# Kernel tuning notes

Hardware: AMD Instinct MI355X
Metric: run time of the kernel (lower is better)

Reference implementation:

```python
import jax, jax.numpy as jnp
import numpy as np

C_IN, C_P1, C_G1, N_OUT = 512, 256, 256, 6
B, H, W = 256, 19, 19


def mish(x):
    return x * jnp.tanh(jax.nn.softplus(x))


def setup_inputs() -> dict:
    key = jax.random.key(0)
    ks = jax.random.split(key, 8)
    x = jax.random.normal(ks[0], (B, C_IN, H, W), dtype=jnp.float32)
    mask = jnp.ones((B, 1, H, W), dtype=jnp.float32)
    conv1p_w = jax.random.normal(ks[1], (C_P1, C_IN), dtype=jnp.float32) * (1.0 / np.sqrt(C_IN))
    conv1g_w = jax.random.normal(ks[2], (C_G1, C_IN), dtype=jnp.float32) * (1.0 / np.sqrt(C_IN))
    beta_g = jnp.zeros((C_G1,), dtype=jnp.float32)
    linear_g_w = jax.random.normal(ks[3], (C_P1, 3 * C_G1), dtype=jnp.float32) * (1.0 / np.sqrt(3 * C_G1))
    beta2 = jnp.zeros((C_P1,), dtype=jnp.float32)
    conv2p_w = jax.random.normal(ks[4], (N_OUT, C_P1), dtype=jnp.float32) * (0.3 / np.sqrt(C_P1))
    return {"x": x, "mask": mask, "conv1p_w": conv1p_w, "conv1g_w": conv1g_w,
            "beta_g": beta_g, "linear_g_w": linear_g_w, "beta2": beta2, "conv2p_w": conv2p_w}


def reference(x, mask, conv1p_w, conv1g_w, beta_g, linear_g_w, beta2, conv2p_w):
    # 1x1 convs are channel GEMMs
    outp = jnp.einsum('bchw,oc->bohw', x, conv1p_w)              # [B, C_P1, H, W]
    outg = jnp.einsum('bchw,oc->bohw', x, conv1g_w)              # [B, C_G1, H, W]
    # BiasMask (scale=None) + Mish
    outg = mish((outg + beta_g[None, :, None, None]) * mask)
    # KataGPool: mean, scaled mean, max (masked)
    mask_sum_hw = jnp.sum(mask, axis=(2, 3), keepdims=True)      # [B,1,1,1]
    layer_mean = jnp.sum(outg * mask, axis=(2, 3), keepdims=True) / mask_sum_hw
    layer_max = jnp.max(outg + (mask - 1.0), axis=(2, 3), keepdims=True)
    sqrt_off = (jnp.sqrt(mask_sum_hw) - 14.0) / 10.0
    pooled = jnp.concatenate([layer_mean, layer_mean * sqrt_off, layer_max], axis=1)  # [B, 3*C_G1, 1, 1]
    pooled = pooled[:, :, 0, 0]                                  # [B, 3*C_G1]
    g = pooled @ linear_g_w.T                                    # [B, C_P1]
    # broadcast-add, BiasMask, Mish
    outp = mish((outp + g[:, :, None, None] + beta2[None, :, None, None]) * mask)
    # final 1x1 conv + invalid-move penalty
    outp = jnp.einsum('bchw,oc->bohw', outp, conv2p_w)           # [B, 6, H, W]
    outp = outp - (1.0 - mask) * 5000.0
    return outp.reshape(outp.shape[0], outp.shape[1], -1)        # [B, 6, H*W]
```

## Files before the change

kernel.cpp:

```cpp
#include <hip/hip_runtime.h>
#include <math.h>

#define BATCH 256
#define CIN   512
#define CP    256
#define HW    361
#define NOUT  6
#define NT    6

typedef short bf16x8 __attribute__((ext_vector_type(8)));
typedef float f32x4  __attribute__((ext_vector_type(4)));

__device__ __forceinline__ short f2bf(float f) {
    unsigned u = __float_as_uint(f);
    u += 0x7fffu + ((u >> 16) & 1u);
    return (short)(u >> 16);
}
__device__ __forceinline__ float bf2f(short s) {
    return __uint_as_float(((unsigned)(unsigned short)s) << 16);
}
__device__ __forceinline__ float mish_f(float v) {
    float u = __expf(v);
    float a = 1.f + u;
    float w = a * a;
    float r = v * (w - 1.f) * __builtin_amdgcn_rcpf(w + 1.f);
    return (v > 30.f) ? v : r;
}
__device__ __forceinline__ void gl_lds16(const void* g, void* l) {
    __builtin_amdgcn_global_load_lds(
        (const __attribute__((address_space(1))) void*)g,
        (__attribute__((address_space(3))) void*)l, 16, 0, 0);
}

__global__ __launch_bounds__(256) void k0_weights(
    const float* __restrict__ w1p, const float* __restrict__ w1g,
    short* __restrict__ wT)
{
    int g = blockIdx.x * 256 + threadIdx.x;
    int kb  = g >> 11;
    int row = (g >> 2) & 511;
    int s   = g & 3;
    int sc  = s ^ ((row >> 1) & 3);
    const float* src = (row < 256) ? (w1p + (size_t)row * CIN)
                                   : (w1g + (size_t)(row - 256) * CIN);
    int c = kb * 32 + sc * 8;
    float f[8];
    *(float4*)(f)     = *(const float4*)(src + c);
    *(float4*)(f + 4) = *(const float4*)(src + c + 4);
    bf16x8 v;
    #pragma unroll
    for (int i = 0; i < 8; ++i) v[i] = f2bf(f[i]);
    *(bf16x8*)((char*)wT + (size_t)kb * 32768 + row * 64 + s * 16) = v;
}

__global__ __launch_bounds__(512, 4) void k1_conv1(
    const float* __restrict__ x, const short* __restrict__ wT,
    const float* __restrict__ mask, const float* __restrict__ beta_g,
    short* __restrict__ outp_pre, float* __restrict__ psum, float* __restrict__ pmax)
{
    int orig = blockIdx.x;
    int newid = (orig & 7) * 192 + (orig >> 3);
    int n = newid % NT;
    int b = newid / NT;

    const int tid = threadIdx.x;
    const int lane = tid & 63, wid = tid >> 6;
    const int lc = lane & 15, lg = lane >> 4;
    const int hw0 = n * 64;

    __shared__ __align__(16) short As[2][16384];
    __shared__ __align__(16) short Bs[2][2048];
    __shared__ float maskS[64];
    __shared__ float betaS[256];

    if (tid < 64) {
        int hwg_ = hw0 + tid;
        maskS[tid] = (hwg_ < HW) ? mask[b * HW + hwg_] : 0.f;
    }
    if (tid < 256) betaS[tid] = beta_g[tid];
    asm volatile("s_waitcnt vmcnt(0) lgkmcnt(0)" ::: "memory");
    __builtin_amdgcn_sched_barrier(0);

    const bool bduty = tid < 256;
    const int brow = tid & 63;
    const int bs   = (tid >> 6) & 3;
    const int hwg  = hw0 + brow;
    const bool bvalid = bduty && (hwg < HW);
    const float* xb = x + ((size_t)b * CIN + bs * 8) * HW + hwg;
    const int bDstOff = brow * 64 + ((bs ^ ((brow >> 1) & 3)) * 16);
    char* bDstBase = (char*)Bs;

    const char* aSrc = (const char*)wT + tid * 16;
    char* aDst = (char*)As + tid * 16;

    int aOff[4], bOff[4];
    #pragma unroll
    for (int mf = 0; mf < 4; ++mf) {
        int r = wid * 64 + mf * 16 + lc;
        aOff[mf] = r * 64 + ((lg ^ ((r >> 1) & 3)) * 16);
    }
    #pragma unroll
    for (int nf = 0; nf < 4; ++nf) {
        int r = nf * 16 + lc;
        bOff[nf] = r * 64 + ((lg ^ ((r >> 1) & 3)) * 16);
    }

    float regB[8];
    #pragma unroll
    for (int i = 0; i < 8; ++i) regB[i] = 0.f;

    f32x4 acc[4][4];
    #pragma unroll
    for (int i = 0; i < 4; ++i)
        #pragma unroll
        for (int j = 0; j < 4; ++j)
            acc[i][j] = (f32x4){0.f, 0.f, 0.f, 0.f};

#define BLOAD(kb)                                                          \
    do {                                                                   \
        if (bduty) {                                                       \
            const float* src_ = xb + (size_t)(kb) * 32 * HW;               \
            _Pragma("unroll")                                              \
            for (int i_ = 0; i_ < 8; ++i_)                                 \
                regB[i_] = bvalid ? src_[(size_t)i_ * HW] : 0.f;           \
        }                                                                  \
    } while (0)

#define BWRITE(buf)                                                        \
    do {                                                                   \
        if (bduty) {                                                       \
            bf16x8 o_;                                                     \
            _Pragma("unroll")                                              \
            for (int i_ = 0; i_ < 8; ++i_) o_[i_] = f2bf(regB[i_]);        \
            *(bf16x8*)(bDstBase + (buf) * 4096 + bDstOff) = o_;            \
        }                                                                  \
    } while (0)

#define ALOAD(buf, kb)                                                     \
    do {                                                                   \
        _Pragma("unroll")                                                  \
        for (int l_ = 0; l_ < 4; ++l_)                                     \
            gl_lds16(aSrc + (size_t)(kb) * 32768 + l_ * 8192,              \
                     aDst + (buf) * 32768 + l_ * 8192);                    \
    } while (0)

    BLOAD(0);
    ALOAD(0, 0);
    asm volatile("s_waitcnt vmcnt(4)" ::: "memory");
    __builtin_amdgcn_sched_barrier(0);
    BWRITE(0);
    asm volatile("s_waitcnt vmcnt(0) lgkmcnt(0)" ::: "memory");
    __builtin_amdgcn_s_barrier();
    __builtin_amdgcn_sched_barrier(0);

    #pragma unroll
    for (int t = 0; t < 16; ++t) {
        const char* ab = (const char*)As + (t & 1) * 32768;
        const char* bb = (const char*)Bs + (t & 1) * 4096;

        bf16x8 aF[4], bF[4];
        #pragma unroll
        for (int mf = 0; mf < 4; ++mf) aF[mf] = *(const bf16x8*)(ab + aOff[mf]);
        #pragma unroll
        for (int nf = 0; nf < 4; ++nf) bF[nf] = *(const bf16x8*)(bb + bOff[nf]);

        if (t < 15) {
            BLOAD(t + 1);
            ALOAD((t + 1) & 1, t + 1);
        }

        __builtin_amdgcn_s_setprio(1);
        #pragma unroll
        for (int mf = 0; mf < 4; ++mf)
            #pragma unroll
            for (int nf = 0; nf < 4; ++nf)
                acc[mf][nf] = __builtin_amdgcn_mfma_f32_16x16x32_bf16(
                    aF[mf], bF[nf], acc[mf][nf], 0, 0, 0);
        __builtin_amdgcn_s_setprio(0);

        if (t < 15) {
            asm volatile("s_waitcnt vmcnt(4)" ::: "memory");
            __builtin_amdgcn_sched_barrier(0);
            BWRITE((t + 1) & 1);
            asm volatile("s_waitcnt vmcnt(0) lgkmcnt(0)" ::: "memory");
            __builtin_amdgcn_s_barrier();
            __builtin_amdgcn_sched_barrier(0);
        }
    }

    if (wid < 4) {
        #pragma unroll
        for (int mf = 0; mf < 4; ++mf) {
            int ch = wid * 64 + mf * 16 + lg * 4;
            #pragma unroll
            for (int nf = 0; nf < 4; ++nf) {
                int hw = hw0 + nf * 16 + lc;
                if (hw < HW) {
                    #pragma unroll
                    for (int j = 0; j < 4; ++j)
                        outp_pre[((size_t)(b * CP + ch + j)) * HW + hw] = f2bf(acc[mf][nf][j]);
                }
            }
        }
    } else {
        #pragma unroll
        for (int mf = 0; mf < 4; ++mf) {
            #pragma unroll
            for (int j = 0; j < 4; ++j) {
                int rloc = (wid - 4) * 64 + mf * 16 + lg * 4 + j;
                float beta = betaS[rloc];
                float s = 0.f, mx = -INFINITY;
                #pragma unroll
                for (int nf = 0; nf < 4; ++nf) {
                    int cl = nf * 16 + lc;
                    int hw = hw0 + cl;
                    float mv = maskS[cl];
                    float val = mish_f((acc[mf][nf][j] + beta) * mv);
                    if (hw < HW) {
                        s += val * mv;
                        mx = fmaxf(mx, val + mv - 1.f);
                    }
                }
                #pragma unroll
                for (int off = 1; off < 16; off <<= 1) {
                    s += __shfl_xor(s, off, 64);
                    mx = fmaxf(mx, __shfl_xor(mx, off, 64));
                }
                if (lc == 0) {
                    psum[((size_t)(b * CP + rloc)) * NT + n] = s;
                    pmax[((size_t)(b * CP + rloc)) * NT + n] = mx;
                }
            }
        }
    }
#undef BLOAD
#undef BWRITE
#undef ALOAD
}

__global__ __launch_bounds__(256) void k2_pool_linear(
    const float* __restrict__ mask, const float* __restrict__ psum,
    const float* __restrict__ pmax, const float* __restrict__ lw,
    float* __restrict__ g_out)
{
    int b = blockIdx.x, t = threadIdx.x;
    __shared__ float pooled[768];
    __shared__ float msr[4];

    float s = 0.f;
    for (int i = t; i < HW; i += 256) s += mask[b * HW + i];
    #pragma unroll
    for (int off = 1; off < 64; off <<= 1) s += __shfl_xor(s, off, 64);
    if ((t & 63) == 0) msr[t >> 6] = s;
    __syncthreads();
    float msum = msr[0] + msr[1] + msr[2] + msr[3];

    {
        int c = t;
        const float* ps = psum + (size_t)(b * CP + c) * NT;
        const float* pm = pmax + (size_t)(b * CP + c) * NT;
        float s3 = 0.f, m3 = -INFINITY;
        #pragma unroll
        for (int i = 0; i < NT; ++i) { s3 += ps[i]; m3 = fmaxf(m3, pm[i]); }
        float mean = s3 / msum;
        float sq = (sqrtf(msum) - 14.f) * 0.1f;
        pooled[c] = mean; pooled[256 + c] = mean * sq; pooled[512 + c] = m3;
    }
    __syncthreads();
    {
        int o = t;
        const float4* wrow = (const float4*)(lw + (size_t)o * 768);
        float acc = 0.f;
        #pragma unroll 8
        for (int j = 0; j < 192; ++j) {
            float4 w4 = wrow[j];
            float4 p4 = *(const float4*)&pooled[j * 4];
            acc += p4.x * w4.x + p4.y * w4.y + p4.z * w4.z + p4.w * w4.w;
        }
        g_out[b * CP + o] = acc;
    }
}

__global__ __launch_bounds__(256) void k3_final(
    const short* __restrict__ outp_pre, const float* __restrict__ mask,
    const float* __restrict__ g_out, const float* __restrict__ beta2,
    const float* __restrict__ w2, float* __restrict__ out)
{
    int ht = blockIdx.x, b = blockIdx.y;
    int t = threadIdx.x;
    __shared__ float w2S[NOUT * 256];
    __shared__ float gbS[256];
    __shared__ float part[NOUT][256];

    for (int i = t; i < NOUT * 256; i += 256) w2S[i] = w2[i];
    gbS[t] = g_out[b * CP + t] + beta2[t];
    __syncthreads();

    int hw = t & 63, cg = t >> 6;
    int hwg = ht * 64 + hw;
    bool valid = hwg < HW;
    float maskv = valid ? mask[b * HW + hwg] : 0.f;

    float acc[NOUT] = {0.f, 0.f, 0.f, 0.f, 0.f, 0.f};
    const short* src = outp_pre + ((size_t)(b * CP + cg * 64)) * HW + hwg;
    #pragma unroll 4
    for (int ci = 0; ci < 64; ++ci) {
        float v = valid ? bf2f(src[(size_t)ci * HW]) : 0.f;
        float mm = mish_f((v + gbS[cg * 64 + ci]) * maskv);
        #pragma unroll
        for (int o = 0; o < NOUT; ++o) acc[o] += mm * w2S[o * 256 + cg * 64 + ci];
    }
    #pragma unroll
    for (int o = 0; o < NOUT; ++o) part[o][t] = acc[o];
    __syncthreads();

    for (int idx = t; idx < NOUT * 64; idx += 256) {
        int o = idx >> 6, h2 = idx & 63;
        int hg = ht * 64 + h2;
        if (hg < HW) {
            float mv = mask[b * HW + hg];
            float sum = part[o][h2] + part[o][64 + h2] + part[o][128 + h2] + part[o][192 + h2];
            out[((size_t)(b * NOUT + o)) * HW + hg] = sum - (1.f - mv) * 5000.f;
        }
    }
}

extern "C" void kernel_launch(void* const* d_in, const int* in_sizes, int n_in,
                              void* d_out, int out_size, void* d_ws, size_t ws_size,
                              hipStream_t stream) {
    const float* x     = (const float*)d_in[0];
    const float* mask  = (const float*)d_in[1];
    const float* w1p   = (const float*)d_in[2];
    const float* w1g   = (const float*)d_in[3];
    const float* betag = (const float*)d_in[4];
    const float* lw    = (const float*)d_in[5];
    const float* beta2 = (const float*)d_in[6];
    const float* w2    = (const float*)d_in[7];
    float* out = (float*)d_out;

    char* ws = (char*)d_ws;
    short* outp_pre = (short*)(ws);
    short* wT       = (short*)(ws + 47316992);
    float* psum     = (float*)(ws + 47841280);
    float* pmax     = (float*)(ws + 49414144);
    float* g_out    = (float*)(ws + 50987008);

    hipLaunchKernelGGL(k0_weights, dim3(128), dim3(256), 0, stream, w1p, w1g, wT);
    hipLaunchKernelGGL(k1_conv1, dim3(1536), dim3(512), 0, stream,
                       x, wT, mask, betag, outp_pre, psum, pmax);
    hipLaunchKernelGGL(k2_pool_linear, dim3(BATCH), dim3(256), 0, stream,
                       mask, psum, pmax, lw, g_out);
    hipLaunchKernelGGL(k3_final, dim3(6, BATCH), dim3(256), 0, stream,
                       outp_pre, mask, g_out, beta2, w2, out);
    (void)in_sizes; (void)n_in; (void)out_size; (void)ws_size;
}
```

Before: 145.5 us.

## Spread x loads across all waves and prefetch B tile two steps ahead

Each of the eight waves now loads four fp32 input channels for the B tile, where before only the first four waves loaded eight each. Register double-buffering lets the global x loads run two k-steps ahead of their LDS write, so the barrier no longer waits on all outstanding loads each iteration. The aim is to hide global load latency for the strided x reads behind the MFMA work. The cost is more registers and a more intricate vmcnt accounting, which must stay correct across the A loads that go directly into LDS.

```diff
diff --git a/kernel.cpp b/kernel.cpp
--- a/kernel.cpp
+++ b/kernel.cpp
@@ -9,6 +9,7 @@
 #define NT    6
 
 typedef short bf16x8 __attribute__((ext_vector_type(8)));
+typedef short bf16x4 __attribute__((ext_vector_type(4)));
 typedef float f32x4  __attribute__((ext_vector_type(4)));
 
 __device__ __forceinline__ short f2bf(float f) {
@@ -81,13 +82,12 @@
     asm volatile("s_waitcnt vmcnt(0) lgkmcnt(0)" ::: "memory");
     __builtin_amdgcn_sched_barrier(0);
 
-    const bool bduty = tid < 256;
     const int brow = tid & 63;
-    const int bs   = (tid >> 6) & 3;
+    const int q    = tid >> 6;
     const int hwg  = hw0 + brow;
-    const bool bvalid = bduty && (hwg < HW);
-    const float* xb = x + ((size_t)b * CIN + bs * 8) * HW + hwg;
-    const int bDstOff = brow * 64 + ((bs ^ ((brow >> 1) & 3)) * 16);
+    const bool bvalid = hwg < HW;
+    const float* xq = x + ((size_t)b * CIN + q * 4) * HW + hwg;
+    const int bDstOff = brow * 64 + (((q >> 1) ^ ((brow >> 1) & 3)) * 16) + ((q & 1) * 8);
     char* bDstBase = (char*)Bs;
 
     const char* aSrc = (const char*)wT + tid * 16;
@@ -105,9 +105,9 @@
         bOff[nf] = r * 64 + ((lg ^ ((r >> 1) & 3)) * 16);
     }
 
-    float regB[8];
-    #pragma unroll
-    for (int i = 0; i < 8; ++i) regB[i] = 0.f;
+    float regB[2][4];
+    #pragma unroll
+    for (int i = 0; i < 4; ++i) { regB[0][i] = 0.f; regB[1][i] = 0.f; }
 
     f32x4 acc[4][4];
     #pragma unroll
@@ -116,24 +116,20 @@
         for (int j = 0; j < 4; ++j)
             acc[i][j] = (f32x4){0.f, 0.f, 0.f, 0.f};
 
-#define BLOAD(kb)                                                          \
+#define BLOAD(SET, kb)                                                     \
     do {                                                                   \
-        if (bduty) {                                                       \
-            const float* src_ = xb + (size_t)(kb) * 32 * HW;               \
-            _Pragma("unroll")                                              \
-            for (int i_ = 0; i_ < 8; ++i_)                                 \
-                regB[i_] = bvalid ? src_[(size_t)i_ * HW] : 0.f;           \
-        }                                                                  \
+        const float* src_ = xq + (size_t)(kb) * 32 * HW;                   \
+        _Pragma("unroll")                                                  \
+        for (int i_ = 0; i_ < 4; ++i_)                                     \
+            regB[SET][i_] = bvalid ? src_[(size_t)i_ * HW] : 0.f;          \
     } while (0)
 
-#define BWRITE(buf)                                                        \
+#define BWRITE(SET, buf)                                                   \
     do {                                                                   \
-        if (bduty) {                                                       \
-            bf16x8 o_;                                                     \
-            _Pragma("unroll")                                              \
-            for (int i_ = 0; i_ < 8; ++i_) o_[i_] = f2bf(regB[i_]);        \
-            *(bf16x8*)(bDstBase + (buf) * 4096 + bDstOff) = o_;            \
-        }                                                                  \
+        bf16x4 o_;                                                         \
+        _Pragma("unroll")                                                  \
+        for (int i_ = 0; i_ < 4; ++i_) o_[i_] = f2bf(regB[SET][i_]);       \
+        *(bf16x4*)(bDstBase + (buf) * 4096 + bDstOff) = o_;                \
     } while (0)
 
 #define ALOAD(buf, kb)                                                     \
@@ -144,12 +140,15 @@
                      aDst + (buf) * 32768 + l_ * 8192);                    \
     } while (0)
 
-    BLOAD(0);
+    BLOAD(0, 0);
     ALOAD(0, 0);
     asm volatile("s_waitcnt vmcnt(4)" ::: "memory");
     __builtin_amdgcn_sched_barrier(0);
-    BWRITE(0);
-    asm volatile("s_waitcnt vmcnt(0) lgkmcnt(0)" ::: "memory");
+    BWRITE(0, 0);
+    BLOAD(1, 1);
+    asm volatile("s_waitcnt vmcnt(4)" ::: "memory");
+    __builtin_amdgcn_sched_barrier(0);
+    asm volatile("s_waitcnt lgkmcnt(0)" ::: "memory");
     __builtin_amdgcn_s_barrier();
     __builtin_amdgcn_sched_barrier(0);
 
@@ -164,10 +163,8 @@
         #pragma unroll
         for (int nf = 0; nf < 4; ++nf) bF[nf] = *(const bf16x8*)(bb + bOff[nf]);
 
-        if (t < 15) {
-            BLOAD(t + 1);
-            ALOAD((t + 1) & 1, t + 1);
-        }
+        if (t < 15) ALOAD((t + 1) & 1, t + 1);
+        if (t < 14) BLOAD(t & 1, t + 2);
 
         __builtin_amdgcn_s_setprio(1);
         #pragma unroll
@@ -179,10 +176,14 @@
         __builtin_amdgcn_s_setprio(0);
 
         if (t < 15) {
-            asm volatile("s_waitcnt vmcnt(4)" ::: "memory");
+            if (t < 14) {
+                asm volatile("s_waitcnt vmcnt(4)" ::: "memory");
+            } else {
+                asm volatile("s_waitcnt vmcnt(0)" ::: "memory");
+            }
             __builtin_amdgcn_sched_barrier(0);
-            BWRITE((t + 1) & 1);
-            asm volatile("s_waitcnt vmcnt(0) lgkmcnt(0)" ::: "memory");
+            BWRITE((t + 1) & 1, (t + 1) & 1);
+            asm volatile("s_waitcnt lgkmcnt(0)" ::: "memory");
             __builtin_amdgcn_s_barrier();
             __builtin_amdgcn_sched_barrier(0);
         }
```

Result: faster. 141.7 us (median of 4 runs) (-2.6%).

## Load conv1 weights directly into registers and widen K tile to 64

Applied to the files above, without the earlier changes.

The conv1 GEMM stops staging the weight (A) tile in LDS via global_load_lds and instead has each wave read its weight fragments straight from global memory into registers, with a simpler row-major weight layout. The x (B) tile now covers 64 input channels per step, loaded by all 512 threads into a larger swizzled LDS buffer, which halves the number of K iterations and barriers. The intent is to free LDS, cut barrier and LDS traffic, and rely on L2 reuse of the weights. The trade-off is that weight loads go through registers with higher latency exposure and more redundant global reads across blocks.

```diff
diff --git a/kernel.cpp b/kernel.cpp
--- a/kernel.cpp
+++ b/kernel.cpp
@@ -26,31 +26,24 @@
     float r = v * (w - 1.f) * __builtin_amdgcn_rcpf(w + 1.f);
     return (v > 30.f) ? v : r;
 }
-__device__ __forceinline__ void gl_lds16(const void* g, void* l) {
-    __builtin_amdgcn_global_load_lds(
-        (const __attribute__((address_space(1))) void*)g,
-        (__attribute__((address_space(3))) void*)l, 16, 0, 0);
-}
 
 __global__ __launch_bounds__(256) void k0_weights(
     const float* __restrict__ w1p, const float* __restrict__ w1g,
     short* __restrict__ wT)
 {
     int g = blockIdx.x * 256 + threadIdx.x;
-    int kb  = g >> 11;
-    int row = (g >> 2) & 511;
-    int s   = g & 3;
-    int sc  = s ^ ((row >> 1) & 3);
+    int row = g >> 6;
+    int ck  = g & 63;
     const float* src = (row < 256) ? (w1p + (size_t)row * CIN)
                                    : (w1g + (size_t)(row - 256) * CIN);
-    int c = kb * 32 + sc * 8;
+    int c = ck * 8;
     float f[8];
     *(float4*)(f)     = *(const float4*)(src + c);
     *(float4*)(f + 4) = *(const float4*)(src + c + 4);
     bf16x8 v;
     #pragma unroll
     for (int i = 0; i < 8; ++i) v[i] = f2bf(f[i]);
-    *(bf16x8*)((char*)wT + (size_t)kb * 32768 + row * 64 + s * 16) = v;
+    *(bf16x8*)((char*)wT + (size_t)row * 1024 + ck * 16) = v;
 }
 
 __global__ __launch_bounds__(512, 4) void k1_conv1(
@@ -68,8 +61,7 @@
     const int lc = lane & 15, lg = lane >> 4;
     const int hw0 = n * 64;
 
-    __shared__ __align__(16) short As[2][16384];
-    __shared__ __align__(16) short Bs[2][2048];
+    __shared__ __align__(16) short Bs[2][4096];
     __shared__ float maskS[64];
     __shared__ float betaS[256];
 
@@ -78,31 +70,24 @@
         maskS[tid] = (hwg_ < HW) ? mask[b * HW + hwg_] : 0.f;
     }
     if (tid < 256) betaS[tid] = beta_g[tid];
-    asm volatile("s_waitcnt vmcnt(0) lgkmcnt(0)" ::: "memory");
-    __builtin_amdgcn_sched_barrier(0);
-
-    const bool bduty = tid < 256;
+
     const int brow = tid & 63;
-    const int bs   = (tid >> 6) & 3;
+    const int q    = tid >> 6;
     const int hwg  = hw0 + brow;
-    const bool bvalid = bduty && (hwg < HW);
-    const float* xb = x + ((size_t)b * CIN + bs * 8) * HW + hwg;
-    const int bDstOff = brow * 64 + ((bs ^ ((brow >> 1) & 3)) * 16);
+    const bool bvalid = hwg < HW;
+    const float* xq = x + ((size_t)b * CIN + q * 8) * HW + hwg;
+    const int bDstOff = brow * 128 + ((q ^ ((brow >> 1) & 7)) * 16);
     char* bDstBase = (char*)Bs;
 
-    const char* aSrc = (const char*)wT + tid * 16;
-    char* aDst = (char*)As + tid * 16;
-
-    int aOff[4], bOff[4];
-    #pragma unroll
-    for (int mf = 0; mf < 4; ++mf) {
-        int r = wid * 64 + mf * 16 + lc;
-        aOff[mf] = r * 64 + ((lg ^ ((r >> 1) & 3)) * 16);
-    }
+    const char* aBase = (const char*)wT + (size_t)(wid * 64 + lc) * 1024 + lg * 16;
+
+    int bOff[4][2];
     #pragma unroll
     for (int nf = 0; nf < 4; ++nf) {
         int r = nf * 16 + lc;
-        bOff[nf] = r * 64 + ((lg ^ ((r >> 1) & 3)) * 16);
+        #pragma unroll
+        for (int kh = 0; kh < 2; ++kh)
+            bOff[nf][kh] = r * 128 + (((kh * 4 + lg) ^ ((r >> 1) & 7)) * 16);
     }
 
     float regB[8];
@@ -118,71 +103,65 @@
 
 #define BLOAD(kb)                                                          \
     do {                                                                   \
-        if (bduty) {                                                       \
-            const float* src_ = xb + (size_t)(kb) * 32 * HW;               \
-            _Pragma("unroll")                                              \
-            for (int i_ = 0; i_ < 8; ++i_)                                 \
-                regB[i_] = bvalid ? src_[(size_t)i_ * HW] : 0.f;           \
-        }                                                                  \
+        const float* src_ = xq + (size_t)(kb) * 64 * HW;                   \
+        _Pragma("unroll")                                                  \
+        for (int i_ = 0; i_ < 8; ++i_)                                     \
+            regB[i_] = bvalid ? src_[(size_t)i_ * HW] : 0.f;               \
     } while (0)
 
 #define BWRITE(buf)                                                        \
     do {                                                                   \
-        if (bduty) {                                                       \
-            bf16x8 o_;                                                     \
+        bf16x8 o_;                                                         \
+        _Pragma("unroll")                                                  \
+        for (int i_ = 0; i_ < 8; ++i_) o_[i_] = f2bf(regB[i_]);            \
+        *(bf16x8*)(bDstBase + (buf) * 8192 + bDstOff) = o_;                \
+    } while (0)
+
+#define ALOAD(dst, kb, kh)                                                 \
+    do {                                                                   \
+        _Pragma("unroll")                                                  \
+        for (int mf_ = 0; mf_ < 4; ++mf_)                                  \
+            dst[mf_] = *(const bf16x8*)(aBase + mf_ * 16384 +              \
+                                        (kb) * 128 + (kh) * 64);           \
+    } while (0)
+
+#define MFMA_HALF(af, buf, kh)                                             \
+    do {                                                                   \
+        bf16x8 bF_[4];                                                     \
+        _Pragma("unroll")                                                  \
+        for (int nf_ = 0; nf_ < 4; ++nf_)                                  \
+            bF_[nf_] = *(const bf16x8*)((const char*)Bs + (buf) * 8192 +   \
+                                        bOff[nf_][kh]);                    \
+        __builtin_amdgcn_s_setprio(1);                                     \
+        _Pragma("unroll")                                                  \
+        for (int mf_ = 0; mf_ < 4; ++mf_)                                  \
             _Pragma("unroll")                                              \
-            for (int i_ = 0; i_ < 8; ++i_) o_[i_] = f2bf(regB[i_]);        \
-            *(bf16x8*)(bDstBase + (buf) * 4096 + bDstOff) = o_;            \
-        }                                                                  \
+            for (int nf_ = 0; nf_ < 4; ++nf_)                              \
+                acc[mf_][nf_] = __builtin_amdgcn_mfma_f32_16x16x32_bf16(   \
+                    af[mf_], bF_[nf_], acc[mf_][nf_], 0, 0, 0);            \
+        __builtin_amdgcn_s_setprio(0);                                     \
     } while (0)
 
-#define ALOAD(buf, kb)                                                     \
-    do {                                                                   \
-        _Pragma("unroll")                                                  \
-        for (int l_ = 0; l_ < 4; ++l_)                                     \
-            gl_lds16(aSrc + (size_t)(kb) * 32768 + l_ * 8192,              \
-                     aDst + (buf) * 32768 + l_ * 8192);                    \
-    } while (0)
-
+    bf16x8 aF0[4], aF1[4];
     BLOAD(0);
-    ALOAD(0, 0);
-    asm volatile("s_waitcnt vmcnt(4)" ::: "memory");
-    __builtin_amdgcn_sched_barrier(0);
     BWRITE(0);
-    asm volatile("s_waitcnt vmcnt(0) lgkmcnt(0)" ::: "memory");
-    __builtin_amdgcn_s_barrier();
-    __builtin_amdgcn_sched_barrier(0);
-
-    #pragma unroll
-    for (int t = 0; t < 16; ++t) {
-        const char* ab = (const char*)As + (t & 1) * 32768;
-        const char* bb = (const char*)Bs + (t & 1) * 4096;
-
-        bf16x8 aF[4], bF[4];
-        #pragma unroll
-        for (int mf = 0; mf < 4; ++mf) aF[mf] = *(const bf16x8*)(ab + aOff[mf]);
-        #pragma unroll
-        for (int nf = 0; nf < 4; ++nf) bF[nf] = *(const bf16x8*)(bb + bOff[nf]);
-
-        if (t < 15) {
-            BLOAD(t + 1);
-            ALOAD((t + 1) & 1, t + 1);
-        }
-
-        __builtin_amdgcn_s_setprio(1);
-        #pragma unroll
-        for (int mf = 0; mf < 4; ++mf)
-            #pragma unroll
-            for (int nf = 0; nf < 4; ++nf)
-                acc[mf][nf] = __builtin_amdgcn_mfma_f32_16x16x32_bf16(
-                    aF[mf], bF[nf], acc[mf][nf], 0, 0, 0);
-        __builtin_amdgcn_s_setprio(0);
-
-        if (t < 15) {
-            asm volatile("s_waitcnt vmcnt(4)" ::: "memory");
+    BLOAD(1);
+    ALOAD(aF0, 0, 0);
+    __syncthreads();
+
+    #pragma unroll
+    for (int t = 0; t < 8; ++t) {
+        const int buf = t & 1;
+        if (t < 7) {  }
+        MFMA_HALF(aF0, buf, 0);
+        ALOAD(aF1, t, 1);
+        MFMA_HALF(aF1, buf, 1);
+        if (t < 7) {
+            BWRITE((t + 1) & 1);
+            if (t < 6) BLOAD(t + 2);
+            ALOAD(aF0, t + 1, 0);
+            asm volatile("s_waitcnt lgkmcnt(0)" ::: "memory");
             __builtin_amdgcn_sched_barrier(0);
-            BWRITE((t + 1) & 1);
-            asm volatile("s_waitcnt vmcnt(0) lgkmcnt(0)" ::: "memory");
             __builtin_amdgcn_s_barrier();
             __builtin_amdgcn_sched_barrier(0);
         }
@@ -236,6 +215,7 @@
 #undef BLOAD
 #undef BWRITE
 #undef ALOAD
+#undef MFMA_HALF
 }
 
 __global__ __launch_bounds__(256) void k2_pool_linear(
```

After: 204.7 us. +40.7%, slower.
